# Kernel tuning notes

Measured on AMD Instinct MI355X. Metric: run time of the kernel, lower is better.

## Reference

```python
import jax, jax.numpy as jnp
import numpy as np
import math

D = 768      # d_model
H = 12       # heads
DH = D // H  # per-head dim
HID = 3072   # ffn hidden
L = 6        # layers each for encoder/decoder
S = 1024     # encoder seq len
T = 1024     # decoder seq len
MAXLEN = 1024


def pos_encoding(d, length):
    # pe[pos, 2i] = sin(pos / scale**i), pe[pos, 2i+1] = cos(pos / scale**i), scale = 1000**(2/d)
    scale = 1000.0 ** (2.0 / d)
    inv = scale ** (-np.arange(d // 2, dtype=np.float64))
    ang = np.arange(length, dtype=np.float64)[:, None] * inv[None, :]
    pe = np.zeros((length, d), dtype=np.float32)
    pe[:, 0::2] = np.sin(ang)
    pe[:, 1::2] = np.cos(ang)
    return jnp.asarray(pe)


def setup_inputs() -> dict:
    key = jax.random.key(0)
    ks = iter(jax.random.split(key, 64))
    def nrm(shape, s=0.02):
        return jax.random.normal(next(ks), shape, dtype=jnp.float32) * s
    inp = {
        'xl': nrm((S, D), 1.0),
        'dl': nrm((T, D), 1.0),
        'pos_enc': pos_encoding(D, MAXLEN),
        # encoder params (stacked over L layers, heads stacked over H)
        'enc_wq': nrm((L, H, DH, D)), 'enc_wk': nrm((L, H, DH, D)), 'enc_wv': nrm((L, H, DH, D)),
        'enc_wo': nrm((L, D, D)), 'enc_bo': jnp.zeros((L, D), jnp.float32),
        'enc_ln_a': jnp.ones((L, 2, D), jnp.float32), 'enc_ln_b': jnp.zeros((L, 2, D), jnp.float32),
        'enc_w1': nrm((L, HID, D)), 'enc_b1': jnp.zeros((L, HID), jnp.float32),
        'enc_w2': nrm((L, D, HID)), 'enc_b2': jnp.zeros((L, D), jnp.float32),
        # decoder self-attention
        'dec_wq': nrm((L, H, DH, D)), 'dec_wk': nrm((L, H, DH, D)), 'dec_wv': nrm((L, H, DH, D)),
        'dec_wo': nrm((L, D, D)), 'dec_bo': jnp.zeros((L, D), jnp.float32),
        # decoder cross-attention
        'dec_cwq': nrm((L, H, DH, D)), 'dec_cwk': nrm((L, H, DH, D)), 'dec_cwv': nrm((L, H, DH, D)),
        'dec_cwo': nrm((L, D, D)), 'dec_cbo': jnp.zeros((L, D), jnp.float32),
        'dec_ln_a': jnp.ones((L, 3, D), jnp.float32), 'dec_ln_b': jnp.zeros((L, 3, D), jnp.float32),
        'dec_w1': nrm((L, HID, D)), 'dec_b1': jnp.zeros((L, HID), jnp.float32),
        'dec_w2': nrm((L, D, HID)), 'dec_b2': jnp.zeros((L, D), jnp.float32),
    }
    return inp


def _ln_res(x, fx, a, b, eps=1e-6):
    # x = x + fx; a*(x-mean)/(std+eps)+b with UNBIASED std (torch default) and std (not var) in denom
    x = x + fx
    m = x.mean(-1, keepdims=True)
    s = jnp.std(x, axis=-1, keepdims=True, ddof=1)
    return a * (x - m) / (s + eps) + b


def _mha(qx, kx, vx, wq, wk, wv, wo, bo, mask=None):
    q = jnp.einsum('sd,hed->hse', qx, wq)  # [H,S,dh]
    k = jnp.einsum('td,hed->hte', kx, wk)
    v = jnp.einsum('td,hed->hte', vx, wv)
    scores = jnp.einsum('hse,hte->hst', q, k) / math.sqrt(q.shape[-1])
    if mask is not None:
        scores = scores + mask
    p = jax.nn.softmax(scores, axis=-1)  # softmax over keys (torch dim=1 on 2D scores)
    o = jnp.einsum('hst,hte->hse', p, v)
    o = jnp.transpose(o, (1, 0, 2)).reshape(qx.shape[0], -1)  # concat heads
    return o @ wo.T + bo


def _ffn(x, w1, b1, w2, b2):
    return jax.nn.relu(x @ w1.T + b1) @ w2.T + b2


def reference(xl, dl, pos_enc, enc_wq, enc_wk, enc_wv, enc_wo, enc_bo, enc_ln_a, enc_ln_b,
              enc_w1, enc_b1, enc_w2, enc_b2,
              dec_wq, dec_wk, dec_wv, dec_wo, dec_bo,
              dec_cwq, dec_cwk, dec_cwv, dec_cwo, dec_cbo,
              dec_ln_a, dec_ln_b, dec_w1, dec_b1, dec_w2, dec_b2):
    m = xl + pos_enc[: xl.shape[0]]
    for l in range(L):
        fx = _mha(m, m, m, enc_wq[l], enc_wk[l], enc_wv[l], enc_wo[l], enc_bo[l])
        m = _ln_res(m, fx, enc_ln_a[l, 0], enc_ln_b[l, 0])
        fx = _ffn(m, enc_w1[l], enc_b1[l], enc_w2[l], enc_b2[l])
        m = _ln_res(m, fx, enc_ln_a[l, 1], enc_ln_b[l, 1])
    n = dl.shape[0]
    # additive causal mask: -10000 where j > i
    cmask = -10000.0 * (jnp.arange(n)[None, :] > jnp.arange(n)[:, None]).astype(jnp.float32)
    out = dl + pos_enc[:n]
    for l in range(L):
        fx = _mha(out, out, out, dec_wq[l], dec_wk[l], dec_wv[l], dec_wo[l], dec_bo[l], cmask)
        out = _ln_res(out, fx, dec_ln_a[l, 0], dec_ln_b[l, 0])
        fx = _mha(out, m, m, dec_cwq[l], dec_cwk[l], dec_cwv[l], dec_cwo[l], dec_cbo[l])
        out = _ln_res(out, fx, dec_ln_a[l, 1], dec_ln_b[l, 1])
        fx = _ffn(out, dec_w1[l], dec_b1[l], dec_w2[l], dec_b2[l])
        out = _ln_res(out, fx, dec_ln_a[l, 2], dec_ln_b[l, 2])
    return jax.nn.softmax(out, axis=1)
```

## Files before the change

### kernel.cpp

```cpp
#include <hip/hip_runtime.h>
#include <math.h>

#define DMODEL 768
#define NHEAD 12
#define DHEAD 64
#define HIDDEN 3072
#define NLAYER 6
#define SEQ 1024
#define AC_ELEMS (SEQ * DMODEL)

typedef unsigned short u16;
typedef __attribute__((ext_vector_type(8))) short short8;
typedef __attribute__((ext_vector_type(4))) float f32x4;

__device__ __forceinline__ u16 f2bf(float f) {
    union { float f; unsigned u; } v; v.f = f;
    unsigned u = v.u;
    return (u16)((u + 0x7fffu + ((u >> 16) & 1u)) >> 16);
}
__device__ __forceinline__ float bf2f(u16 b) {
    union { unsigned u; float f; } v; v.u = ((unsigned)b) << 16; return v.f;
}

__device__ __forceinline__ void async16(const void* g, void* l) {
    __builtin_amdgcn_global_load_lds(
        (const __attribute__((address_space(1))) unsigned int*)g,
        (__attribute__((address_space(3))) unsigned int*)l, 16, 0, 0);
}

template<int N> __device__ __forceinline__ void waitv() {
    asm volatile("s_waitcnt vmcnt(%0)" :: "n"(N) : "memory");
    __builtin_amdgcn_sched_barrier(0);
}
__device__ __forceinline__ void drain_all() {
    asm volatile("s_waitcnt vmcnt(0) lgkmcnt(0)" ::: "memory");
    __builtin_amdgcn_sched_barrier(0);
}
__device__ __forceinline__ void bar() {
    __builtin_amdgcn_sched_barrier(0);
    __builtin_amdgcn_s_barrier();
    __builtin_amdgcn_sched_barrier(0);
}

__device__ __forceinline__ float block_sum(float v, float* red) {
    int tid = threadIdx.x;
    red[tid] = v;
    __syncthreads();
#pragma unroll
    for (int s = 128; s > 0; s >>= 1) {
        if (tid < s) red[tid] += red[tid + s];
        __syncthreads();
    }
    float r = red[0];
    __syncthreads();
    return r;
}
__device__ __forceinline__ float block_max(float v, float* red) {
    int tid = threadIdx.x;
    red[tid] = v;
    __syncthreads();
#pragma unroll
    for (int s = 128; s > 0; s >>= 1) {
        if (tid < s) red[tid] = fmaxf(red[tid], red[tid + s]);
        __syncthreads();
    }
    float r = red[0];
    __syncthreads();
    return r;
}

__global__ __launch_bounds__(256) void add_pe(const float* __restrict__ a,
                                              const float* __restrict__ b,
                                              float* __restrict__ o,
                                              u16* __restrict__ ob, int n) {
    int i = blockIdx.x * 256 + threadIdx.x;
    if (i < n) { float v = a[i] + b[i]; o[i] = v; ob[i] = f2bf(v); }
}

__global__ __launch_bounds__(256) void cvt_bf16(const float* __restrict__ src,
                                                u16* __restrict__ dst,
                                                long long per, long long sls, long long dls) {
    long long i = ((long long)blockIdx.x * 256 + threadIdx.x) * 4;
    if (i >= per) return;
    const float* s = src + (long long)blockIdx.y * sls + i;
    u16* d = dst + (long long)blockIdx.y * dls + i;
    float4 v = *(const float4*)s;
    ushort4 o;
    o.x = f2bf(v.x); o.y = f2bf(v.y); o.z = f2bf(v.z); o.w = f2bf(v.w);
    *(ushort4*)d = o;
}

template<int TM, int TN, int WR, int WC>
__global__ __launch_bounds__(WR * WC * 64) void gemm_mfma(
    const u16* __restrict__ A, int lda,
    const void* __restrict__ Bp, int ldb, int b_f32,
    const float* __restrict__ bias,
    void* __restrict__ Cp, int ldc, int c_bf16,
    float* __restrict__ C2,
    u16* __restrict__ vt_out, int vt_col0, int vt_mode,
    int Ksub, int relu)
{
    constexpr int T  = WR * WC * 64;
    constexpr bool MW = (WR * WC) > 1;
    constexpr int FM = TM / (WR * 16), FN = TN / (WC * 16);
    constexpr int NA = TM * 8 / T, NB = TN * 8 / T;
    constexpr int LPS = NA + NB;
    __shared__ __align__(16) u16 As[3][TM * 64];
    __shared__ __align__(16) u16 Bs[3][TN * 64];

    const int zs = blockIdx.z;
    const u16*   B16 = (const u16*)Bp   + (long long)zs * Ksub;
    const float* B32 = (const float*)Bp + (long long)zs * Ksub;
    A += (long long)zs * Ksub;
    u16*   C16 = (u16*)Cp;
    float* C32 = (float*)Cp;

    const int t = threadIdx.x, lane = t & 63, w = t >> 6;
    const int wy = w / WC, wx = w % WC;
    const int n0 = blockIdx.y * TM, m0 = blockIdx.x * TN;

    auto stage = [&](int b, int k0) {
#pragma unroll
        for (int i = 0; i < NA; ++i) {
            int L = i * T + t;
            int row = L >> 3, cp = L & 7, c = cp ^ (row & 7);
            async16(A + (long long)(n0 + row) * lda + k0 + (c << 3),
                    &As[b][(i * T + w * 64) * 8]);
        }
        if (!b_f32) {
#pragma unroll
            for (int i = 0; i < NB; ++i) {
                int L = i * T + t;
                int row = L >> 3, cp = L & 7, c = cp ^ (row & 7);
                async16(B16 + (long long)(m0 + row) * ldb + k0 + (c << 3),
                        &Bs[b][(i * T + w * 64) * 8]);
            }
        } else {
#pragma unroll
            for (int i = 0; i < NB; ++i) {
                int L = i * T + t;
                int row = L >> 3, cp = L & 7, c = cp ^ (row & 7);
                const float* s = B32 + (long long)(m0 + row) * ldb + k0 + (c << 3);
                float4 x = *(const float4*)s;
                float4 y = *(const float4*)(s + 4);
                uint4 pk;
                pk.x = (unsigned)f2bf(x.x) | ((unsigned)f2bf(x.y) << 16);
                pk.y = (unsigned)f2bf(x.z) | ((unsigned)f2bf(x.w) << 16);
                pk.z = (unsigned)f2bf(y.x) | ((unsigned)f2bf(y.y) << 16);
                pk.w = (unsigned)f2bf(y.z) | ((unsigned)f2bf(y.w) << 16);
                *(uint4*)&Bs[b][row * 64 + cp * 8] = pk;
            }
        }
    };

    const int nk = Ksub / 64;
    stage(0, 0);
    if (nk > 1) stage(1, 64);

    f32x4 acc[FM][FN] = {};

    for (int tt = 0; tt < nk; ++tt) {
        if (tt + 2 < nk) stage((tt + 2) % 3, (tt + 2) * 64);
        if (b_f32)             drain_all();
        else if (tt + 2 < nk)  waitv<2 * LPS>();
        else if (tt + 1 < nk)  waitv<LPS>();
        else                   waitv<0>();
        if (MW) bar();

        const u16* Ac = As[tt % 3];
        const u16* Bc = Bs[tt % 3];
#pragma unroll
        for (int kk = 0; kk < 2; ++kk) {
            short8 af[FM], bfv[FN];
            const int cb = kk * 4 + (lane >> 4);
#pragma unroll
            for (int m = 0; m < FM; ++m) {
                int R = wy * (TM / WR) + m * 16 + (lane & 15);
                af[m] = *(const short8*)&Ac[R * 64 + ((cb ^ (R & 7)) << 3)];
            }
#pragma unroll
            for (int n = 0; n < FN; ++n) {
                int R = wx * (TN / WC) + n * 16 + (lane & 15);
                bfv[n] = *(const short8*)&Bc[R * 64 + ((cb ^ (R & 7)) << 3)];
            }
#pragma unroll
            for (int m = 0; m < FM; ++m)
#pragma unroll
                for (int n = 0; n < FN; ++n)
                    acc[m][n] = __builtin_amdgcn_mfma_f32_16x16x32_bf16(af[m], bfv[n], acc[m][n], 0, 0, 0);
        }
        if (MW) bar();
    }

    const int cj = lane & 15, ci0 = (lane >> 4) << 2;
    const bool z0 = (zs == 0);
    float* C2z = C2 + (long long)(zs - 1) * AC_ELEMS;
#pragma unroll
    for (int m = 0; m < FM; ++m) {
#pragma unroll
        for (int n = 0; n < FN; ++n) {
            int col = m0 + wx * (TN / WC) + n * 16 + cj;
            float bv = (z0 && bias) ? bias[col] : 0.0f;
            long long vtidx = -1;
            if (z0 && vt_mode == 1 && col >= vt_col0) vtidx = (long long)(col - vt_col0) * SEQ;
            else if (z0 && vt_mode == 2) {
                int blk = col / 1536, rem = col % 1536;
                if (rem >= 768) vtidx = ((long long)blk * 768 + rem - 768) * SEQ;
            }
#pragma unroll
            for (int r = 0; r < 4; ++r) {
                int row = n0 + wy * (TM / WR) + m * 16 + ci0 + r;
                float v = acc[m][n][r] + bv;
                if (relu) v = fmaxf(v, 0.0f);
                if (!z0)             C2z[(long long)row * ldc + col] = v;
                else if (vtidx >= 0) vt_out[vtidx + row] = f2bf(v);
                else if (c_bf16)     C16[(long long)row * ldc + col] = f2bf(v);
                else                 C32[(long long)row * ldc + col] = v;
            }
        }
    }
}

template<int CAUSAL>
__global__ __launch_bounds__(256) void attn_split(
    const u16* __restrict__ Qg, int ldq,
    const u16* __restrict__ Kg, int ldk,
    const u16* __restrict__ VT,
    float* __restrict__ Op,
    float* __restrict__ Ml)
{
    const int h  = blockIdx.y;
    const int qt = blockIdx.x;
    const int s  = blockIdx.z;
    const int q0 = qt * 64;
    const int t = threadIdx.x, lane = t & 63, w = t >> 6;

    const int last = CAUSAL ? qt : (SEQ / 64 - 1);

    if (CAUSAL && s > last) {
        for (int e = t; e < 64 * 64; e += 256) {
            int r = e >> 6, c = e & 63;
            Op[(long long)s * AC_ELEMS + (long long)(q0 + r) * DMODEL + h * 64 + c] = 0.0f;
        }
        if (t < 64) {
            long long mi = (((long long)s * NHEAD + h) * SEQ + q0 + t) * 2;
            Ml[mi] = -3.0e38f; Ml[mi + 1] = 0.0f;
        }
        return;
    }

    __shared__ __align__(16) u16 Ks[2][64 * 64];
    __shared__ __align__(16) u16 Vs[2][64 * 64];
    __shared__ __align__(16) u16 Ps[4][16 * 64];

    short8 qf[2];
    {
        int qrow = q0 + w * 16 + (lane & 15);
        const u16* qp = Qg + (long long)qrow * ldq + h * DHEAD + ((lane >> 4) << 3);
        qf[0] = *(const short8*)qp;
        qf[1] = *(const short8*)(qp + 32);
    }

    auto stage = [&](int b, int kt) {
#pragma unroll
        for (int i = 0; i < 2; ++i) {
            int LL = i * 256 + t;
            int row = LL >> 3, cp = LL & 7, c = cp ^ (row & 7);
            async16(Kg + (long long)(kt * 64 + row) * ldk + h * DHEAD + (c << 3),
                    &Ks[b][(i * 256 + w * 64) * 8]);
            async16(VT + (long long)(h * DHEAD + row) * SEQ + kt * 64 + (c << 3),
                    &Vs[b][(i * 256 + w * 64) * 8]);
        }
    };

    f32x4 o_acc[4] = {};
    float m_r[4], l_r[4];
#pragma unroll
    for (int r = 0; r < 4; ++r) { m_r[r] = -3.0e38f; l_r[r] = 0.f; }

    stage(0, s);

    int buf = 0;
    for (int kt = s; kt <= last; kt += 2) {
        if (kt + 2 <= last) { stage(buf ^ 1, kt + 2); waitv<4>(); }
        else                { waitv<0>(); }
        bar();

        f32x4 sv[4] = {};
#pragma unroll
        for (int kk = 0; kk < 2; ++kk) {
            const int cb = kk * 4 + (lane >> 4);
#pragma unroll
            for (int n = 0; n < 4; ++n) {
                int R = n * 16 + (lane & 15);
                short8 kf = *(const short8*)&Ks[buf][R * 64 + ((cb ^ (R & 7)) << 3)];
                sv[n] = __builtin_amdgcn_mfma_f32_16x16x32_bf16(qf[kk], kf, sv[n], 0, 0, 0);
            }
        }

#pragma unroll
        for (int n = 0; n < 4; ++n) {
            int keyl = n * 16 + (lane & 15);
#pragma unroll
            for (int r = 0; r < 4; ++r) {
                float v = sv[n][r] * 0.125f;
                if (CAUSAL && kt == qt) {
                    int ql = w * 16 + ((lane >> 4) << 2) + r;
                    if (keyl > ql) v -= 10000.0f;
                }
                sv[n][r] = v;
            }
        }

#pragma unroll
        for (int r = 0; r < 4; ++r) {
            float vm = fmaxf(fmaxf(sv[0][r], sv[1][r]), fmaxf(sv[2][r], sv[3][r]));
            vm = fmaxf(vm, __shfl_xor(vm, 1));
            vm = fmaxf(vm, __shfl_xor(vm, 2));
            vm = fmaxf(vm, __shfl_xor(vm, 4));
            vm = fmaxf(vm, __shfl_xor(vm, 8));
            float mn = fmaxf(m_r[r], vm);
            float sf = __expf(m_r[r] - mn);
            m_r[r] = mn;
            float rowsum = 0.f;
#pragma unroll
            for (int n = 0; n < 4; ++n) {
                float p = __expf(sv[n][r] - mn);
                sv[n][r] = p;
                rowsum += p;
            }
            rowsum += __shfl_xor(rowsum, 1);
            rowsum += __shfl_xor(rowsum, 2);
            rowsum += __shfl_xor(rowsum, 4);
            rowsum += __shfl_xor(rowsum, 8);
            l_r[r] = l_r[r] * sf + rowsum;
#pragma unroll
            for (int d = 0; d < 4; ++d) o_acc[d][r] *= sf;
        }

#pragma unroll
        for (int n = 0; n < 4; ++n) {
            int jh = lane & 7;
            int chunk = n * 2 + ((lane & 15) >> 3);
#pragma unroll
            for (int r = 0; r < 4; ++r) {
                int q = ((lane >> 4) << 2) + r;
                Ps[w][q * 64 + ((chunk ^ (q & 7)) << 3) + jh] = f2bf(sv[n][r]);
            }
        }

#pragma unroll
        for (int kk = 0; kk < 2; ++kk) {
            int q = lane & 15;
            int chunk = (lane >> 4) + kk * 4;
            short8 pf = *(const short8*)&Ps[w][q * 64 + ((chunk ^ (q & 7)) << 3)];
            const int cb = kk * 4 + (lane >> 4);
#pragma unroll
            for (int d = 0; d < 4; ++d) {
                int R = d * 16 + (lane & 15);
                short8 vf = *(const short8*)&Vs[buf][R * 64 + ((cb ^ (R & 7)) << 3)];
                o_acc[d] = __builtin_amdgcn_mfma_f32_16x16x32_bf16(pf, vf, o_acc[d], 0, 0, 0);
            }
        }
        bar();
        buf ^= 1;
    }

#pragma unroll
    for (int r = 0; r < 4; ++r) {
        int row = q0 + w * 16 + ((lane >> 4) << 2) + r;
#pragma unroll
        for (int d = 0; d < 4; ++d) {
            int col = h * DHEAD + d * 16 + (lane & 15);
            Op[(long long)s * AC_ELEMS + (long long)row * DMODEL + col] = o_acc[d][r];
        }
        if ((lane & 15) == 0) {
            long long mi = (((long long)s * NHEAD + h) * SEQ + row) * 2;
            Ml[mi] = m_r[r]; Ml[mi + 1] = l_r[r];
        }
    }
}

__global__ __launch_bounds__(192) void attn_combine(const float* __restrict__ Op,
                                                    const float* __restrict__ Ml,
                                                    u16* __restrict__ O) {
    const int row = blockIdx.x;
    const int c0 = threadIdx.x * 4;
    const int h = c0 >> 6;
    long long m0i = (((long long)0 * NHEAD + h) * SEQ + row) * 2;
    long long m1i = (((long long)1 * NHEAD + h) * SEQ + row) * 2;
    float m0 = Ml[m0i], l0 = Ml[m0i + 1];
    float m1 = Ml[m1i], l1 = Ml[m1i + 1];
    float M = fmaxf(m0, m1);
    float w0 = __expf(m0 - M), w1 = __expf(m1 - M);
    float inv = 1.0f / (w0 * l0 + w1 * l1);
    float4 a = *(const float4*)&Op[(long long)row * DMODEL + c0];
    float4 b = *(const float4*)&Op[(long long)AC_ELEMS + (long long)row * DMODEL + c0];
    ushort4 o;
    o.x = f2bf((w0 * a.x + w1 * b.x) * inv);
    o.y = f2bf((w0 * a.y + w1 * b.y) * inv);
    o.z = f2bf((w0 * a.z + w1 * b.z) * inv);
    o.w = f2bf((w0 * a.w + w1 * b.w) * inv);
    *(ushort4*)&O[(long long)row * DMODEL + c0] = o;
}

__global__ __launch_bounds__(256) void softmax_f32(const float* __restrict__ in,
                                                   float* __restrict__ out, int width) {
    const float* row = in + (long long)blockIdx.x * width;
    float* orow = out + (long long)blockIdx.x * width;
    int tid = threadIdx.x;
    __shared__ float red[256];
    int nf4 = width >> 2;
    float4 v = {-1e30f, -1e30f, -1e30f, -1e30f};
    if (tid < nf4) v = ((const float4*)row)[tid];
    float mx = fmaxf(fmaxf(v.x, v.y), fmaxf(v.z, v.w));
    mx = block_max(mx, red);
    float4 e = {0.f, 0.f, 0.f, 0.f};
    float s = 0.f;
    if (tid < nf4) {
        e.x = __expf(v.x - mx); e.y = __expf(v.y - mx);
        e.z = __expf(v.z - mx); e.w = __expf(v.w - mx);
        s = e.x + e.y + e.z + e.w;
    }
    s = block_sum(s, red);
    float inv = 1.0f / s;
    if (tid < nf4) {
        e.x *= inv; e.y *= inv; e.z *= inv; e.w *= inv;
        ((float4*)orow)[tid] = e;
    }
}

__global__ __launch_bounds__(256) void ln_res_kernel(float* __restrict__ x,
                                                     const float* __restrict__ fx,
                                                     const float* __restrict__ fx2,
                                                     int n2,
                                                     const float* __restrict__ ga,
                                                     const float* __restrict__ gb,
                                                     u16* __restrict__ xb) {
    long long row = blockIdx.x;
    float* xr = x + row * DMODEL;
    const float* fr = fx + row * DMODEL;
    u16* xbr = xb + row * DMODEL;
    int tid = threadIdx.x;
    __shared__ float red[256];

    float4 tv = {0.f, 0.f, 0.f, 0.f};
    if (tid < 192) {
        float4 a = ((const float4*)xr)[tid];
        float4 f = ((const float4*)fr)[tid];
        tv.x = a.x + f.x; tv.y = a.y + f.y; tv.z = a.z + f.z; tv.w = a.w + f.w;
        for (int j = 0; j < n2; ++j) {
            float4 g = ((const float4*)(fx2 + (long long)j * AC_ELEMS + row * DMODEL))[tid];
            tv.x += g.x; tv.y += g.y; tv.z += g.z; tv.w += g.w;
        }
    }
    float sum = tv.x + tv.y + tv.z + tv.w;
    sum = block_sum(sum, red);
    float mean = sum * (1.0f / (float)DMODEL);

    float4 d = {0.f, 0.f, 0.f, 0.f};
    float ss = 0.f;
    if (tid < 192) {
        d.x = tv.x - mean; d.y = tv.y - mean; d.z = tv.z - mean; d.w = tv.w - mean;
        ss = d.x * d.x + d.y * d.y + d.z * d.z + d.w * d.w;
    }
    ss = block_sum(ss, red);
    float stdv = sqrtf(ss / (float)(DMODEL - 1));
    float inv = 1.0f / (stdv + 1e-6f);

    if (tid < 192) {
        float4 A = ((const float4*)ga)[tid];
        float4 B = ((const float4*)gb)[tid];
        float4 o;
        o.x = A.x * d.x * inv + B.x;
        o.y = A.y * d.y * inv + B.y;
        o.z = A.z * d.z * inv + B.z;
        o.w = A.w * d.w * inv + B.w;
        ((float4*)xr)[tid] = o;
        ushort4 ob;
        ob.x = f2bf(o.x); ob.y = f2bf(o.y); ob.z = f2bf(o.z); ob.w = f2bf(o.w);
        ((ushort4*)xbr)[tid] = ob;
    }
}

struct GArg {
    const u16* A; int lda;
    const void* B; int ldb; int b_f32;
    const float* bias;
    void* C; int ldc; int c_bf16;
    u16* vt; int vt_col0; int vt_mode;
    int N, M, K; int relu;
};
template<int TM, int TN, int WR, int WC>
static inline void glaunch(hipStream_t st, const GArg& a, int splitk = 1, float* C2 = nullptr) {
    dim3 grid(a.M / TN, a.N / TM, splitk);
    hipLaunchKernelGGL((gemm_mfma<TM, TN, WR, WC>), grid, dim3(WR * WC * 64), 0, st,
                       a.A, a.lda, a.B, a.ldb, a.b_f32, a.bias, a.C, a.ldc, a.c_bf16,
                       C2, a.vt, a.vt_col0, a.vt_mode, a.K / splitk, a.relu);
}

extern "C" void kernel_launch(void* const* d_in, const int* in_sizes, int n_in,
                              void* d_out, int out_size, void* d_ws, size_t ws_size,
                              hipStream_t stream) {
    const float* xl      = (const float*)d_in[0];
    const float* dl      = (const float*)d_in[1];
    const float* pe      = (const float*)d_in[2];
    const float* enc_wq  = (const float*)d_in[3];
    const float* enc_wk  = (const float*)d_in[4];
    const float* enc_wv  = (const float*)d_in[5];
    const float* enc_wo  = (const float*)d_in[6];
    const float* enc_bo  = (const float*)d_in[7];
    const float* enc_lna = (const float*)d_in[8];
    const float* enc_lnb = (const float*)d_in[9];
    const float* enc_w1  = (const float*)d_in[10];
    const float* enc_b1  = (const float*)d_in[11];
    const float* enc_w2  = (const float*)d_in[12];
    const float* enc_b2  = (const float*)d_in[13];
    const float* dec_wq  = (const float*)d_in[14];
    const float* dec_wk  = (const float*)d_in[15];
    const float* dec_wv  = (const float*)d_in[16];
    const float* dec_wo  = (const float*)d_in[17];
    const float* dec_bo  = (const float*)d_in[18];
    const float* dec_cwq = (const float*)d_in[19];
    const float* dec_cwk = (const float*)d_in[20];
    const float* dec_cwv = (const float*)d_in[21];
    const float* dec_cwo = (const float*)d_in[22];
    const float* dec_cbo = (const float*)d_in[23];
    const float* dec_lna = (const float*)d_in[24];
    const float* dec_lnb = (const float*)d_in[25];
    const float* dec_w1  = (const float*)d_in[26];
    const float* dec_b1  = (const float*)d_in[27];
    const float* dec_w2  = (const float*)d_in[28];
    const float* dec_b2  = (const float*)d_in[29];

    const long long AC   = AC_ELEMS;
    const long long DD   = (long long)DMODEL * DMODEL;
    const long long WH   = (long long)HIDDEN * DMODEL;
    const long long QKVC = (long long)SEQ * 3 * DMODEL;
    const long long SH   = (long long)SEQ * HIDDEN;

    float* mbuf  = (float*)d_ws;
    float* xbuf  = mbuf + AC;
    float* fbuf  = xbuf + AC;
    float* fbuf2 = fbuf + AC;
    float* Opart = fbuf2 + AC;
    float* Ml    = Opart + 2 * AC;
    u16* u = (u16*)(Ml + 2LL * NHEAD * SEQ * 2);
    u16* mb16 = u;  u += AC;
    u16* xb16 = u;  u += AC;
    u16* qkvb = u;  u += QKVC;
    u16* vt   = u;  u += AC;
    u16* ob   = u;  u += AC;
    u16* hb   = u;  u += SH;
    u16* ckb  = u;  u += 12LL * AC;
    u16* cvb  = u;  u += 6LL * AC;

    u16* W = u;
    long long woff = 0;
    const long long W_ENC_QKV = woff; woff += 18 * DD;
    const long long W_ENC_WO  = woff; woff += 6 * DD;
    const long long W_ENC_W1  = woff; woff += 6 * WH;
    const long long W_ENC_W2  = woff; woff += 6 * WH;
    const long long W_DEC_QKV = woff; woff += 18 * DD;
    const long long W_DEC_CQ  = woff; woff += 6 * DD;
    const long long W_DEC_CKV = woff; woff += 12 * DD;
    const long long W_DEC_WO  = woff; woff += 6 * DD;
    const long long W_DEC_CWO = woff; woff += 6 * DD;
    const long long W_DEC_W1  = woff; woff += 6 * WH;
    const long long W_DEC_W2  = woff; woff += 6 * WH;
    const long long need = (long long)((char*)(W + woff) - (char*)d_ws);
    const bool conv = ((long long)ws_size >= need);

    if (conv) {
        auto cvt = [&](const float* src, long long dst_off, long long per, long long sls, long long dls, int L) {
            dim3 grid((unsigned)((per / 4 + 255) / 256), L);
            hipLaunchKernelGGL(cvt_bf16, grid, dim3(256), 0, stream, src, W + dst_off, per, sls, dls);
        };
        cvt(enc_wq, W_ENC_QKV + 0 * DD, DD, DD, 3 * DD, NLAYER);
        cvt(enc_wk, W_ENC_QKV + 1 * DD, DD, DD, 3 * DD, NLAYER);
        cvt(enc_wv, W_ENC_QKV + 2 * DD, DD, DD, 3 * DD, NLAYER);
        cvt(enc_wo, W_ENC_WO, 6 * DD, 0, 0, 1);
        cvt(enc_w1, W_ENC_W1, 6 * WH, 0, 0, 1);
        cvt(enc_w2, W_ENC_W2, 6 * WH, 0, 0, 1);
        cvt(dec_wq, W_DEC_QKV + 0 * DD, DD, DD, 3 * DD, NLAYER);
        cvt(dec_wk, W_DEC_QKV + 1 * DD, DD, DD, 3 * DD, NLAYER);
        cvt(dec_wv, W_DEC_QKV + 2 * DD, DD, DD, 3 * DD, NLAYER);
        cvt(dec_cwq, W_DEC_CQ, 6 * DD, 0, 0, 1);
        cvt(dec_cwk, W_DEC_CKV + 0 * DD, DD, DD, 2 * DD, NLAYER);
        cvt(dec_cwv, W_DEC_CKV + 1 * DD, DD, DD, 2 * DD, NLAYER);
        cvt(dec_wo, W_DEC_WO, 6 * DD, 0, 0, 1);
        cvt(dec_cwo, W_DEC_CWO, 6 * DD, 0, 0, 1);
        cvt(dec_w1, W_DEC_W1, 6 * WH, 0, 0, 1);
        cvt(dec_w2, W_DEC_W2, 6 * WH, 0, 0, 1);
    }

    hipLaunchKernelGGL(add_pe, dim3((int)(AC / 256)), dim3(256), 0, stream, xl, pe, mbuf, mb16, (int)AC);

    auto attn = [&](int causal, const u16* Qg, int ldq, const u16* Kg, int ldk, const u16* VT) {
        dim3 grid(SEQ / 64, NHEAD, 2);
        if (causal)
            hipLaunchKernelGGL((attn_split<1>), grid, dim3(256), 0, stream, Qg, ldq, Kg, ldk, VT, Opart, Ml);
        else
            hipLaunchKernelGGL((attn_split<0>), grid, dim3(256), 0, stream, Qg, ldq, Kg, ldk, VT, Opart, Ml);
        hipLaunchKernelGGL(attn_combine, dim3(SEQ), dim3(192), 0, stream, Opart, Ml, ob);
    };

    for (int l = 0; l < NLAYER; ++l) {
        if (conv) {
            GArg qkv = { mb16, DMODEL, W + W_ENC_QKV + l * 3 * DD, DMODEL, 0, nullptr,
                         qkvb, 3 * DMODEL, 1, vt, 2 * DMODEL, 1,
                         SEQ, 3 * DMODEL, DMODEL, 0 };
            glaunch<64, 64, 2, 2>(stream, qkv);
        } else {
            const float* wps[3] = { enc_wq + l * DD, enc_wk + l * DD, enc_wv + l * DD };
            for (int j = 0; j < 3; ++j) {
                GArg a = { mb16, DMODEL, wps[j], DMODEL, 1, nullptr,
                           qkvb + j * DMODEL, 3 * DMODEL, 1,
                           (j == 2) ? vt : nullptr, 0, (j == 2) ? 1 : 0,
                           SEQ, DMODEL, DMODEL, 0 };
                glaunch<32, 32, 1, 1>(stream, a);
            }
        }
        attn(0, qkvb, 3 * DMODEL, qkvb + DMODEL, 3 * DMODEL, vt);
        GArg wo = { ob, DMODEL,
                    conv ? (const void*)(W + W_ENC_WO + l * DD) : (const void*)(enc_wo + l * DD),
                    DMODEL, conv ? 0 : 1, enc_bo + (long long)l * DMODEL,
                    fbuf, DMODEL, 0, nullptr, 0, 0,
                    SEQ, DMODEL, DMODEL, 0 };
        glaunch<32, 32, 1, 1>(stream, wo);
        hipLaunchKernelGGL(ln_res_kernel, dim3(SEQ), dim3(256), 0, stream,
                           mbuf, fbuf, (const float*)nullptr, 0,
                           enc_lna + (long long)(l * 2 + 0) * DMODEL,
                           enc_lnb + (long long)(l * 2 + 0) * DMODEL, mb16);
        GArg f1 = { mb16, DMODEL,
                    conv ? (const void*)(W + W_ENC_W1 + l * WH) : (const void*)(enc_w1 + l * WH),
                    DMODEL, conv ? 0 : 1, enc_b1 + (long long)l * HIDDEN,
                    hb, HIDDEN, 1, nullptr, 0, 0,
                    SEQ, HIDDEN, DMODEL, 1 };
        glaunch<64, 64, 2, 2>(stream, f1);
        GArg f2 = { hb, HIDDEN,
                    conv ? (const void*)(W + W_ENC_W2 + l * WH) : (const void*)(enc_w2 + l * WH),
                    HIDDEN, conv ? 0 : 1, enc_b2 + (long long)l * DMODEL,
                    fbuf, DMODEL, 0, nullptr, 0, 0,
                    SEQ, DMODEL, HIDDEN, 0 };
        glaunch<64, 64, 2, 2>(stream, f2, 2, fbuf2);
        hipLaunchKernelGGL(ln_res_kernel, dim3(SEQ), dim3(256), 0, stream,
                           mbuf, fbuf, fbuf2, 1,
                           enc_lna + (long long)(l * 2 + 1) * DMODEL,
                           enc_lnb + (long long)(l * 2 + 1) * DMODEL, mb16);
    }

    if (conv) {
        GArg ckv = { mb16, DMODEL, W + W_DEC_CKV, DMODEL, 0, nullptr,
                     ckb, 12 * DMODEL, 1, cvb, 0, 2,
                     SEQ, 12 * DMODEL, DMODEL, 0 };
        glaunch<64, 64, 2, 2>(stream, ckv);
    }

    hipLaunchKernelGGL(add_pe, dim3((int)(AC / 256)), dim3(256), 0, stream, dl, pe, xbuf, xb16, (int)AC);

    for (int l = 0; l < NLAYER; ++l) {
        if (conv) {
            GArg qkv = { xb16, DMODEL, W + W_DEC_QKV + l * 3 * DD, DMODEL, 0, nullptr,
                         qkvb, 3 * DMODEL, 1, vt, 2 * DMODEL, 1,
                         SEQ, 3 * DMODEL, DMODEL, 0 };
            glaunch<64, 64, 2, 2>(stream, qkv);
        } else {
            const float* wps[3] = { dec_wq + l * DD, dec_wk + l * DD, dec_wv + l * DD };
            for (int j = 0; j < 3; ++j) {
                GArg a = { xb16, DMODEL, wps[j], DMODEL, 1, nullptr,
                           qkvb + j * DMODEL, 3 * DMODEL, 1,
                           (j == 2) ? vt : nullptr, 0, (j == 2) ? 1 : 0,
                           SEQ, DMODEL, DMODEL, 0 };
                glaunch<32, 32, 1, 1>(stream, a);
            }
        }
        attn(1, qkvb, 3 * DMODEL, qkvb + DMODEL, 3 * DMODEL, vt);
        GArg wo = { ob, DMODEL,
                    conv ? (const void*)(W + W_DEC_WO + l * DD) : (const void*)(dec_wo + l * DD),
                    DMODEL, conv ? 0 : 1, dec_bo + (long long)l * DMODEL,
                    fbuf, DMODEL, 0, nullptr, 0, 0,
                    SEQ, DMODEL, DMODEL, 0 };
        glaunch<32, 32, 1, 1>(stream, wo);
        hipLaunchKernelGGL(ln_res_kernel, dim3(SEQ), dim3(256), 0, stream,
                           xbuf, fbuf, (const float*)nullptr, 0,
                           dec_lna + (long long)(l * 3 + 0) * DMODEL,
                           dec_lnb + (long long)(l * 3 + 0) * DMODEL, xb16);

        if (conv) {
            GArg q = { xb16, DMODEL, W + W_DEC_CQ + l * DD, DMODEL, 0, nullptr,
                       qkvb, 3 * DMODEL, 1, nullptr, 0, 0,
                       SEQ, DMODEL, DMODEL, 0 };
            glaunch<32, 32, 1, 1>(stream, q);
            attn(0, qkvb, 3 * DMODEL, ckb + l * 2 * DMODEL, 12 * DMODEL, cvb + (long long)l * AC);
        } else {
            GArg q = { xb16, DMODEL, dec_cwq + l * DD, DMODEL, 1, nullptr,
                       qkvb, 3 * DMODEL, 1, nullptr, 0, 0,
                       SEQ, DMODEL, DMODEL, 0 };
            glaunch<32, 32, 1, 1>(stream, q);
            GArg ck = { mb16, DMODEL, dec_cwk + l * DD, DMODEL, 1, nullptr,
                        qkvb + DMODEL, 3 * DMODEL, 1, nullptr, 0, 0,
                        SEQ, DMODEL, DMODEL, 0 };
            glaunch<32, 32, 1, 1>(stream, ck);
            GArg cv = { mb16, DMODEL, dec_cwv + l * DD, DMODEL, 1, nullptr,
                        qkvb + 2 * DMODEL, 3 * DMODEL, 1, vt, 0, 1,
                        SEQ, DMODEL, DMODEL, 0 };
            glaunch<32, 32, 1, 1>(stream, cv);
            attn(0, qkvb, 3 * DMODEL, qkvb + DMODEL, 3 * DMODEL, vt);
        }
        GArg cwo = { ob, DMODEL,
                     conv ? (const void*)(W + W_DEC_CWO + l * DD) : (const void*)(dec_cwo + l * DD),
                     DMODEL, conv ? 0 : 1, dec_cbo + (long long)l * DMODEL,
                     fbuf, DMODEL, 0, nullptr, 0, 0,
                     SEQ, DMODEL, DMODEL, 0 };
        glaunch<32, 32, 1, 1>(stream, cwo);
        hipLaunchKernelGGL(ln_res_kernel, dim3(SEQ), dim3(256), 0, stream,
                           xbuf, fbuf, (const float*)nullptr, 0,
                           dec_lna + (long long)(l * 3 + 1) * DMODEL,
                           dec_lnb + (long long)(l * 3 + 1) * DMODEL, xb16);

        GArg f1 = { xb16, DMODEL,
                    conv ? (const void*)(W + W_DEC_W1 + l * WH) : (const void*)(dec_w1 + l * WH),
                    DMODEL, conv ? 0 : 1, dec_b1 + (long long)l * HIDDEN,
                    hb, HIDDEN, 1, nullptr, 0, 0,
                    SEQ, HIDDEN, DMODEL, 1 };
        glaunch<64, 64, 2, 2>(stream, f1);
        GArg f2 = { hb, HIDDEN,
                    conv ? (const void*)(W + W_DEC_W2 + l * WH) : (const void*)(dec_w2 + l * WH),
                    HIDDEN, conv ? 0 : 1, dec_b2 + (long long)l * DMODEL,
                    fbuf, DMODEL, 0, nullptr, 0, 0,
                    SEQ, DMODEL, HIDDEN, 0 };
        glaunch<64, 64, 2, 2>(stream, f2, 2, fbuf2);
        hipLaunchKernelGGL(ln_res_kernel, dim3(SEQ), dim3(256), 0, stream,
                           xbuf, fbuf, fbuf2, 1,
                           dec_lna + (long long)(l * 3 + 2) * DMODEL,
                           dec_lnb + (long long)(l * 3 + 2) * DMODEL, xb16);
    }

    hipLaunchKernelGGL(softmax_f32, dim3(SEQ), dim3(256), 0, stream, xbuf, (float*)d_out, DMODEL);
}
```

Measured before the change: 1.727 ms.

## Replace split-KV attention plus combine with 32-query-row blocks and direct output

Drops the two-way key-split attention kernel and its separate combine pass. Each block now handles 32 query rows with two waves over the full key range, so there are twice as many query tiles. The block normalizes the result in registers and writes bf16 output directly. This removes the fp32 partial-output and max/sum workspace traffic and one kernel launch per attention call. In exchange, each block walks a longer serial key loop and gets less K/V reuse per staged tile.

```diff
diff --git a/kernel.cpp b/kernel.cpp
--- a/kernel.cpp
+++ b/kernel.cpp
@@ -222,40 +222,25 @@
 }
 
 template<int CAUSAL>
-__global__ __launch_bounds__(256) void attn_split(
+__global__ __launch_bounds__(128) void attn_q32(
     const u16* __restrict__ Qg, int ldq,
     const u16* __restrict__ Kg, int ldk,
     const u16* __restrict__ VT,
-    float* __restrict__ Op,
-    float* __restrict__ Ml)
+    u16* __restrict__ O)
 {
     const int h  = blockIdx.y;
     const int qt = blockIdx.x;
-    const int s  = blockIdx.z;
-    const int q0 = qt * 64;
     const int t = threadIdx.x, lane = t & 63, w = t >> 6;
 
-    const int last = CAUSAL ? qt : (SEQ / 64 - 1);
-
-    if (CAUSAL && s > last) {
-        for (int e = t; e < 64 * 64; e += 256) {
-            int r = e >> 6, c = e & 63;
-            Op[(long long)s * AC_ELEMS + (long long)(q0 + r) * DMODEL + h * 64 + c] = 0.0f;
-        }
-        if (t < 64) {
-            long long mi = (((long long)s * NHEAD + h) * SEQ + q0 + t) * 2;
-            Ml[mi] = -3.0e38f; Ml[mi + 1] = 0.0f;
-        }
-        return;
-    }
+    const int last = CAUSAL ? (qt >> 1) : (SEQ / 64 - 1);
 
     __shared__ __align__(16) u16 Ks[2][64 * 64];
     __shared__ __align__(16) u16 Vs[2][64 * 64];
-    __shared__ __align__(16) u16 Ps[4][16 * 64];
+    __shared__ __align__(16) u16 Ps[2][16 * 64];
 
     short8 qf[2];
     {
-        int qrow = q0 + w * 16 + (lane & 15);
+        int qrow = qt * 32 + w * 16 + (lane & 15);
         const u16* qp = Qg + (long long)qrow * ldq + h * DHEAD + ((lane >> 4) << 3);
         qf[0] = *(const short8*)qp;
         qf[1] = *(const short8*)(qp + 32);
@@ -263,13 +248,13 @@
 
     auto stage = [&](int b, int kt) {
 #pragma unroll
-        for (int i = 0; i < 2; ++i) {
-            int LL = i * 256 + t;
+        for (int i = 0; i < 4; ++i) {
+            int LL = i * 128 + t;
             int row = LL >> 3, cp = LL & 7, c = cp ^ (row & 7);
             async16(Kg + (long long)(kt * 64 + row) * ldk + h * DHEAD + (c << 3),
-                    &Ks[b][(i * 256 + w * 64) * 8]);
+                    &Ks[b][(i * 128 + w * 64) * 8]);
             async16(VT + (long long)(h * DHEAD + row) * SEQ + kt * 64 + (c << 3),
-                    &Vs[b][(i * 256 + w * 64) * 8]);
+                    &Vs[b][(i * 128 + w * 64) * 8]);
         }
     };
 
@@ -278,11 +263,11 @@
 #pragma unroll
     for (int r = 0; r < 4; ++r) { m_r[r] = -3.0e38f; l_r[r] = 0.f; }
 
-    stage(0, s);
-
-    int buf = 0;
-    for (int kt = s; kt <= last; kt += 2) {
-        if (kt + 2 <= last) { stage(buf ^ 1, kt + 2); waitv<4>(); }
+    stage(0, 0);
+
+    for (int kt = 0; kt <= last; ++kt) {
+        const int buf = kt & 1;
+        if (kt + 1 <= last) { stage(buf ^ 1, kt + 1); waitv<8>(); }
         else                { waitv<0>(); }
         bar();
 
@@ -304,8 +289,8 @@
 #pragma unroll
             for (int r = 0; r < 4; ++r) {
                 float v = sv[n][r] * 0.125f;
-                if (CAUSAL && kt == qt) {
-                    int ql = w * 16 + ((lane >> 4) << 2) + r;
+                if (CAUSAL && kt == last) {
+                    int ql = (qt & 1) * 32 + w * 16 + ((lane >> 4) << 2) + r;
                     if (keyl > ql) v -= 10000.0f;
                 }
                 sv[n][r] = v;
@@ -363,45 +348,18 @@
             }
         }
         bar();
-        buf ^= 1;
     }
 
 #pragma unroll
     for (int r = 0; r < 4; ++r) {
-        int row = q0 + w * 16 + ((lane >> 4) << 2) + r;
+        float inv = 1.0f / l_r[r];
+        int row = qt * 32 + w * 16 + ((lane >> 4) << 2) + r;
 #pragma unroll
         for (int d = 0; d < 4; ++d) {
             int col = h * DHEAD + d * 16 + (lane & 15);
-            Op[(long long)s * AC_ELEMS + (long long)row * DMODEL + col] = o_acc[d][r];
-        }
-        if ((lane & 15) == 0) {
-            long long mi = (((long long)s * NHEAD + h) * SEQ + row) * 2;
-            Ml[mi] = m_r[r]; Ml[mi + 1] = l_r[r];
-        }
-    }
-}
-
-__global__ __launch_bounds__(192) void attn_combine(const float* __restrict__ Op,
-                                                    const float* __restrict__ Ml,
-                                                    u16* __restrict__ O) {
-    const int row = blockIdx.x;
-    const int c0 = threadIdx.x * 4;
-    const int h = c0 >> 6;
-    long long m0i = (((long long)0 * NHEAD + h) * SEQ + row) * 2;
-    long long m1i = (((long long)1 * NHEAD + h) * SEQ + row) * 2;
-    float m0 = Ml[m0i], l0 = Ml[m0i + 1];
-    float m1 = Ml[m1i], l1 = Ml[m1i + 1];
-    float M = fmaxf(m0, m1);
-    float w0 = __expf(m0 - M), w1 = __expf(m1 - M);
-    float inv = 1.0f / (w0 * l0 + w1 * l1);
-    float4 a = *(const float4*)&Op[(long long)row * DMODEL + c0];
-    float4 b = *(const float4*)&Op[(long long)AC_ELEMS + (long long)row * DMODEL + c0];
-    ushort4 o;
-    o.x = f2bf((w0 * a.x + w1 * b.x) * inv);
-    o.y = f2bf((w0 * a.y + w1 * b.y) * inv);
-    o.z = f2bf((w0 * a.z + w1 * b.z) * inv);
-    o.w = f2bf((w0 * a.w + w1 * b.w) * inv);
-    *(ushort4*)&O[(long long)row * DMODEL + c0] = o;
+            O[(long long)row * DMODEL + col] = f2bf(o_acc[d][r] * inv);
+        }
+    }
 }
 
 __global__ __launch_bounds__(256) void softmax_f32(const float* __restrict__ in,
@@ -543,9 +501,7 @@
     float* xbuf  = mbuf + AC;
     float* fbuf  = xbuf + AC;
     float* fbuf2 = fbuf + AC;
-    float* Opart = fbuf2 + AC;
-    float* Ml    = Opart + 2 * AC;
-    u16* u = (u16*)(Ml + 2LL * NHEAD * SEQ * 2);
+    u16* u = (u16*)(fbuf2 + AC);
     u16* mb16 = u;  u += AC;
     u16* xb16 = u;  u += AC;
     u16* qkvb = u;  u += QKVC;
@@ -597,12 +553,11 @@
     hipLaunchKernelGGL(add_pe, dim3((int)(AC / 256)), dim3(256), 0, stream, xl, pe, mbuf, mb16, (int)AC);
 
     auto attn = [&](int causal, const u16* Qg, int ldq, const u16* Kg, int ldk, const u16* VT) {
-        dim3 grid(SEQ / 64, NHEAD, 2);
+        dim3 grid(SEQ / 32, NHEAD);
         if (causal)
-            hipLaunchKernelGGL((attn_split<1>), grid, dim3(256), 0, stream, Qg, ldq, Kg, ldk, VT, Opart, Ml);
+            hipLaunchKernelGGL((attn_q32<1>), grid, dim3(128), 0, stream, Qg, ldq, Kg, ldk, VT, ob);
         else
-            hipLaunchKernelGGL((attn_split<0>), grid, dim3(256), 0, stream, Qg, ldq, Kg, ldk, VT, Opart, Ml);
-        hipLaunchKernelGGL(attn_combine, dim3(SEQ), dim3(192), 0, stream, Opart, Ml, ob);
+            hipLaunchKernelGGL((attn_q32<0>), grid, dim3(128), 0, stream, Qg, ldq, Kg, ldk, VT, ob);
     };
 
     for (int l = 0; l < NLAYER; ++l) {
```

Measured after the change: 1.840 ms. 1.07x slower.
